# Performance work log

Hardware: AMD Instinct MI355X
Metric: run time of the kernel (lower is better)

The kernel has to match this reference:

```python
import jax, jax.numpy as jnp
import numpy as np

T = 2048      # total tokens (single prefill sequence)
HID = 2048    # hidden_size
H = 16        # num k-heads == num v-heads
DK = 128      # key head dim
DV = 128      # value head dim
K = 4         # causal conv kernel width
EPS = 1e-6


def setup_inputs() -> dict:
    key = jax.random.key(0)
    ks = jax.random.split(key, 10)
    n = lambda k, shape, sc: (jax.random.normal(k, shape, jnp.float32) * sc)
    return {
        "hidden_states": n(ks[0], (T, HID), 1.0),
        "Wq": n(ks[1], (HID, H * DK), 0.02),
        "Wk": n(ks[2], (HID, H * DK), 0.02),
        "Wv": n(ks[3], (HID, H * DV), 0.02),
        "Wb": n(ks[4], (HID, H), 0.02),
        "conv_wq": n(ks[5], (H * DK, K), 0.5),
        "conv_wk": n(ks[6], (H * DK, K), 0.5),
        "conv_wv": n(ks[7], (H * DV, K), 0.5),
        "o_norm_w": jnp.ones((DV,), jnp.float32),
        "Wo": n(ks[8], (HID, HID), 0.02),
    }


def _causal_conv_silu(x, w):
    # x: [T, D], w: [D, K] depthwise causal conv, then SiLU (matches causal_conv1d_fn)
    xp = jnp.pad(x, ((K - 1, 0), (0, 0)))
    y = sum(xp[j:j + T] * w[:, j] for j in range(K))
    return jax.nn.silu(y)


def _l2norm(x):
    return x * jax.lax.rsqrt(jnp.sum(x * x, axis=-1, keepdims=True) + EPS)


def reference(hidden_states, Wq, Wk, Wv, Wb, conv_wq, conv_wk, conv_wv, o_norm_w, Wo):
    # projections [T, H*D]
    q = _causal_conv_silu(hidden_states @ Wq, conv_wq).reshape(T, H, DK)
    k = _causal_conv_silu(hidden_states @ Wk, conv_wk).reshape(T, H, DK)
    v = _causal_conv_silu(hidden_states @ Wv, conv_wv).reshape(T, H, DV)
    beta = jax.nn.sigmoid(hidden_states @ Wb)  # [T, H]

    # qk l2-norm + scale (FLA chunk_delta_rule defaults)
    q = _l2norm(q) * (DK ** -0.5)
    k = _l2norm(k)

    # delta-rule recurrence: S <- S + beta * k (v - k^T S)
    def step(S, inp):
        q_t, k_t, v_t, b_t = inp            # [H,DK],[H,DK],[H,DV],[H]
        kS = jnp.einsum('hk,hkv->hv', k_t, S)
        delta = b_t[:, None] * (v_t - kS)   # [H, DV]
        S = S + jnp.einsum('hk,hv->hkv', k_t, delta)
        o_t = jnp.einsum('hk,hkv->hv', q_t, S)
        return S, o_t

    S0 = jnp.zeros((H, DK, DV), jnp.float32)
    _, o = jax.lax.scan(step, S0, (q, k, v, beta))  # o: [T, H, DV]

    # per-head RMSNorm on value head dim
    o = o * jax.lax.rsqrt(jnp.mean(o * o, axis=-1, keepdims=True) + EPS) * o_norm_w
    out = o.reshape(T, H * DV) @ Wo
    return out
```

## Files before the change

### kernel.cpp

```cpp
#include <hip/hip_runtime.h>

typedef unsigned short u16;
typedef __attribute__((ext_vector_type(4))) unsigned short u16x4;
typedef __attribute__((ext_vector_type(8))) unsigned short u16x8;
typedef __attribute__((ext_vector_type(8))) short short8;
typedef __attribute__((ext_vector_type(4))) float f32x4;

#define DEVI __device__ __forceinline__

DEVI u16 f2b(float f) {
  union { float f; unsigned u; } x; x.f = f;
  unsigned r = (x.u + 0x7fffu + ((x.u >> 16) & 1u)) >> 16;
  return (u16)r;
}
DEVI float b2f(u16 h) {
  union { unsigned u; float f; } x; x.u = ((unsigned)h) << 16;
  return x.f;
}
DEVI f32x4 mfma_bf16(short8 a, short8 b, f32x4 c) {
  return __builtin_amdgcn_mfma_f32_16x16x32_bf16(a, b, c, 0, 0, 0);
}
DEVI void gl2lds16(const u16* g, u16* l) {
  __builtin_amdgcn_global_load_lds((__attribute__((address_space(1))) void*)g,
                                   (__attribute__((address_space(3))) void*)l,
                                   16, 0, 0);
}
DEVI void barrier_lds() {
  asm volatile("s_waitcnt lgkmcnt(0)\n\ts_barrier" ::: "memory");
}

__global__ void k_cvt(const float* __restrict__ src, u16* __restrict__ dst, int n4,
                      const float* __restrict__ Wb, u16* __restrict__ WbT) {
  int b = blockIdx.x;
  if (b < 4096) {
    int i = b * 256 + threadIdx.x;
    if (i < n4) {
      float4 v = ((const float4*)src)[i];
      u16x4 r; r.x = f2b(v.x); r.y = f2b(v.y); r.z = f2b(v.z); r.w = f2b(v.w);
      ((u16x4*)dst)[i] = r;
    }
  } else {
    int j = (b - 4096) * 256 + threadIdx.x;
    int n = j >> 11, k = j & 2047;
    WbT[j] = f2b(Wb[k * 16 + n]);
  }
}

__global__ __launch_bounds__(256)
void k_transpose4(const float* __restrict__ s0, const float* __restrict__ s1,
                  const float* __restrict__ s2, const float* __restrict__ s3,
                  u16* __restrict__ d0, u16* __restrict__ d1,
                  u16* __restrict__ d2, u16* __restrict__ d3) {
  const int RC = 2048;
  const float* src = (blockIdx.z == 0) ? s0 : (blockIdx.z == 1) ? s1 : (blockIdx.z == 2) ? s2 : s3;
  u16* dst = (blockIdx.z == 0) ? d0 : (blockIdx.z == 1) ? d1 : (blockIdx.z == 2) ? d2 : d3;
  __shared__ u16 tile[64 * 66];
  int bx = blockIdx.x << 6, by = blockIdx.y << 6;
  int x = threadIdx.x & 63, g = threadIdx.x >> 6;
#pragma unroll
  for (int i = 0; i < 16; ++i) {
    int r = (i << 2) + g;
    tile[x * 66 + r] = f2b(src[(size_t)(by + r) * RC + bx + x]);
  }
  __syncthreads();
#pragma unroll
  for (int i = 0; i < 16; ++i) {
    int r = (i << 2) + g;
    dst[(size_t)(bx + r) * RC + by + x] = tile[r * 66 + x];
  }
}

__global__ __launch_bounds__(256, 4)
void k_gemm_bt(const u16* __restrict__ A, const u16* __restrict__ BT,
               float* __restrict__ Cf, u16* __restrict__ Cb,
               int M, int N, int K, int outbf) {
  __shared__ __align__(16) u16 As[4096];
  __shared__ __align__(16) u16 Bs[4096];
  const int tid = threadIdx.x, wave = tid >> 6, lane = tid & 63;
  const long bm = (long)blockIdx.y << 7, bn = (long)blockIdx.x << 7;
  const int r0 = (wave << 4) + (lane >> 2);
  const int kof = (((lane & 3) ^ ((lane >> 3) & 3)) << 3);
  const u16* gA = A + (bm + r0) * (long)K + kof;
  const u16* gB = BT + (bn + r0) * (long)K + kof;
  u16* lA = As + (wave << 9);
  u16* lB = Bs + (wave << 9);
  const long stepR = (long)64 * K;
  const int wr = (wave >> 1) << 6, wc = (wave & 1) << 6;
  const int fr = lane & 15, fq = (lane >> 4) << 3;
  const int fqs = fq ^ (((fr >> 1) & 3) << 3);
  f32x4 acc[4][4];
#pragma unroll
  for (int i = 0; i < 4; ++i)
#pragma unroll
    for (int j = 0; j < 4; ++j) acc[i][j] = (f32x4){0.f, 0.f, 0.f, 0.f};
  for (int k0 = 0; k0 < K; k0 += 32) {
    gl2lds16(gA + k0, lA);
    gl2lds16(gA + stepR + k0, lA + 2048);
    gl2lds16(gB + k0, lB);
    gl2lds16(gB + stepR + k0, lB + 2048);
    __syncthreads();
    short8 af[4], bfr[4];
#pragma unroll
    for (int t = 0; t < 4; ++t)
      af[t] = *(const short8*)&As[(wr + (t << 4) + fr) * 32 + fqs];
#pragma unroll
    for (int t = 0; t < 4; ++t)
      bfr[t] = *(const short8*)&Bs[(wc + (t << 4) + fr) * 32 + fqs];
#pragma unroll
    for (int i = 0; i < 4; ++i)
#pragma unroll
      for (int j = 0; j < 4; ++j)
        acc[i][j] = mfma_bf16(af[i], bfr[j], acc[i][j]);
    __syncthreads();
  }
  const int er = (lane >> 4) << 2, ec = lane & 15;
#pragma unroll
  for (int i = 0; i < 4; ++i)
#pragma unroll
    for (int j = 0; j < 4; ++j)
#pragma unroll
      for (int r = 0; r < 4; ++r) {
        long row = bm + wr + (i << 4) + er + r;
        long col = bn + wc + (j << 4) + ec;
        if (outbf) Cb[row * N + col] = f2b(acc[i][j][r]);
        else       Cf[row * N + col] = acc[i][j][r];
      }
}

__global__ __launch_bounds__(256, 4)
void k_gemm_bt64(const u16* __restrict__ A, const u16* __restrict__ BT,
                 float* __restrict__ Cf, int M, int N, int K) {
  __shared__ __align__(16) u16 As[2048];
  __shared__ __align__(16) u16 Bs[4096];
  const int tid = threadIdx.x, wave = tid >> 6, lane = tid & 63;
  const long bm = (long)blockIdx.y << 6, bn = (long)blockIdx.x << 7;
  const int r0 = (wave << 4) + (lane >> 2);
  const int kof = (((lane & 3) ^ ((lane >> 3) & 3)) << 3);
  const u16* gA = A + (bm + r0) * (long)K + kof;
  const u16* gB = BT + (bn + r0) * (long)K + kof;
  u16* lA = As + (wave << 9);
  u16* lB = Bs + (wave << 9);
  const long stepR = (long)64 * K;
  const int wr = (wave >> 1) << 5, wc = (wave & 1) << 6;
  const int fr = lane & 15, fq = (lane >> 4) << 3;
  const int fqs = fq ^ (((fr >> 1) & 3) << 3);
  f32x4 acc[2][4];
#pragma unroll
  for (int i = 0; i < 2; ++i)
#pragma unroll
    for (int j = 0; j < 4; ++j) acc[i][j] = (f32x4){0.f, 0.f, 0.f, 0.f};
  for (int k0 = 0; k0 < K; k0 += 32) {
    gl2lds16(gA + k0, lA);
    gl2lds16(gB + k0, lB);
    gl2lds16(gB + stepR + k0, lB + 2048);
    __syncthreads();
    short8 af[2], bfr[4];
#pragma unroll
    for (int t = 0; t < 2; ++t)
      af[t] = *(const short8*)&As[(wr + (t << 4) + fr) * 32 + fqs];
#pragma unroll
    for (int t = 0; t < 4; ++t)
      bfr[t] = *(const short8*)&Bs[(wc + (t << 4) + fr) * 32 + fqs];
#pragma unroll
    for (int i = 0; i < 2; ++i)
#pragma unroll
      for (int j = 0; j < 4; ++j)
        acc[i][j] = mfma_bf16(af[i], bfr[j], acc[i][j]);
    __syncthreads();
  }
  const int er = (lane >> 4) << 2, ec = lane & 15;
#pragma unroll
  for (int i = 0; i < 2; ++i)
#pragma unroll
    for (int j = 0; j < 4; ++j)
#pragma unroll
      for (int r = 0; r < 4; ++r) {
        long row = bm + wr + (i << 4) + er + r;
        long col = bn + wc + (j << 4) + ec;
        Cf[row * N + col] = acc[i][j][r];
      }
}

__global__ __launch_bounds__(256, 4)
void k_beta(const u16* __restrict__ Xb, const u16* __restrict__ WbT,
            float* __restrict__ beta) {
  __shared__ float part[4][256];
  int tid = threadIdx.x, w = tid >> 6, lane = tid & 63;
  int t0 = blockIdx.x << 4;
  int fr = lane & 15, fq = (lane >> 4) << 3;
  const u16* ap = Xb + (size_t)(t0 + fr) * 2048 + (w << 9) + fq;
  const u16* bp = WbT + (size_t)fr * 2048 + (w << 9) + fq;
  f32x4 acc = {0.f, 0.f, 0.f, 0.f};
#pragma unroll
  for (int ks = 0; ks < 16; ++ks)
    acc = mfma_bf16(*(const short8*)(ap + (ks << 5)), *(const short8*)(bp + (ks << 5)), acc);
  int er = (lane >> 4) << 2;
#pragma unroll
  for (int r = 0; r < 4; ++r) part[w][(er + r) * 16 + fr] = acc[r];
  __syncthreads();
  float s = part[0][tid] + part[1][tid] + part[2][tid] + part[3][tid];
  beta[(t0 << 4) + tid] = 1.f / (1.f + __expf(-s));
}

__global__ void k_conv(const u16* __restrict__ qkv,
                       const float* __restrict__ cwq, const float* __restrict__ cwk,
                       const float* __restrict__ cwv,
                       u16* __restrict__ qn, u16* __restrict__ kn, u16* __restrict__ vn) {
  int t = blockIdx.x, s = blockIdx.y;
  int kind = s >> 4, h = s & 15, d = threadIdx.x;
  int col = kind * 2048 + (h << 7) + d;
  const float* cw = (kind == 0) ? cwq : ((kind == 1) ? cwk : cwv);
  float4 w = *(const float4*)(cw + (size_t)((h << 7) + d) * 4);
  float x[4];
#pragma unroll
  for (int j = 0; j < 4; ++j) {
    int tt = t - 3 + j;
    x[j] = (tt >= 0) ? b2f(qkv[(size_t)tt * 6144 + col]) : 0.f;
  }
  float y = x[0] * w.x + x[1] * w.y + x[2] * w.z + x[3] * w.w;
  y = y / (1.f + __expf(-y));
  float sc = 1.f;
  __shared__ float red[2];
  if (kind < 2) {
    float ss = y * y;
#pragma unroll
    for (int off = 32; off; off >>= 1) ss += __shfl_down(ss, off, 64);
    int lane = threadIdx.x & 63, wv = threadIdx.x >> 6;
    if (lane == 0) red[wv] = ss;
    __syncthreads();
    float tot = red[0] + red[1];
    sc = rsqrtf(tot + 1e-6f);
    if (kind == 0) sc *= 0.08838834764831843f;
  }
  u16* dst = (kind == 0) ? qn : ((kind == 1) ? kn : vn);
  dst[((size_t)h << 18) + ((size_t)t << 7) + d] = f2b(y * sc);
}

__global__ __launch_bounds__(256, 2)
void k_prep(const u16* __restrict__ qn, const u16* __restrict__ kn, const u16* __restrict__ vn,
            const float* __restrict__ beta,
            u16* __restrict__ Gg, u16* __restrict__ Wg,
            u16* __restrict__ KTg, u16* __restrict__ UTg) {
  __shared__ __align__(16) char sm[70912];
  u16*  Kc  = (u16*)sm;
  u16*  Qc  = (u16*)(sm + 17408);
  u16*  Vc  = (u16*)(sm + 34816);
  u16*  KTl = (u16*)(sm + 52224);
  float* AL = (float*)(sm + 52224);
  float* Bl = (float*)(sm + 70656);
  u16*  WR  = Qc;
  int h = blockIdx.x, c = blockIdx.y;
  int tid = threadIdx.x, wave = tid >> 6, lane = tid & 63;
  size_t ch = (size_t)(c * 16 + h);
  const u16* kb = kn + ((size_t)h << 18) + ((size_t)c << 13);
  const u16* qb = qn + ((size_t)h << 18) + ((size_t)c << 13);
  const u16* vb = vn + ((size_t)h << 18) + ((size_t)c << 13);
#pragma unroll
  for (int s = 0; s < 4; ++s) {
    int e = (tid + (s << 8)) << 3;
    int t = e >> 7, d = e & 127;
    *(u16x8*)&Kc[t * 136 + d] = *(const u16x8*)(kb + e);
    *(u16x8*)&Qc[t * 136 + d] = *(const u16x8*)(qb + e);
    *(u16x8*)&Vc[t * 136 + d] = *(const u16x8*)(vb + e);
  }
  if (tid < 64) Bl[tid] = beta[((c << 6) + tid) * 16 + h];
  __syncthreads();
  int fr = lane & 15, fq = (lane >> 4) << 3, q4 = (lane >> 4) << 2;
  int arow = (wave << 4) + fr;
  f32x4 kk[4], qk[4];
#pragma unroll
  for (int ct = 0; ct < 4; ++ct) { kk[ct] = (f32x4){0.f,0.f,0.f,0.f}; qk[ct] = (f32x4){0.f,0.f,0.f,0.f}; }
#pragma unroll
  for (int ks = 0; ks < 4; ++ks) {
    short8 aK = *(const short8*)&Kc[arow * 136 + (ks << 5) + fq];
    short8 aQ = *(const short8*)&Qc[arow * 136 + (ks << 5) + fq];
#pragma unroll
    for (int ct = 0; ct < 4; ++ct) {
      short8 bK = *(const short8*)&Kc[((ct << 4) + fr) * 136 + (ks << 5) + fq];
      kk[ct] = mfma_bf16(aK, bK, kk[ct]);
      qk[ct] = mfma_bf16(aQ, bK, qk[ct]);
    }
  }
#pragma unroll
  for (int ct = 0; ct < 4; ++ct)
#pragma unroll
    for (int r = 0; r < 4; ++r) {
      int i = (wave << 4) + q4 + r, j = (ct << 4) + fr;
      Gg[(ch << 12) + i * 64 + j] = f2b((j <= i) ? qk[ct][r] : 0.f);
    }
  {
    int d = tid & 127, tg = tid >> 7;
#pragma unroll
    for (int it = 0; it < 4; ++it) {
      int t0 = (tg + (it << 1)) << 3;
      u16x8 pk;
#pragma unroll
      for (int j = 0; j < 8; ++j) pk[j] = Kc[(t0 + j) * 136 + d];
      *(u16x8*)&KTl[d * 72 + t0] = pk;
    }
  }
  __syncthreads();
#pragma unroll
  for (int it = 0; it < 4; ++it) {
    int idx = tid + (it << 8);
    int row = idx >> 3, j8 = (idx & 7) << 3;
    *(u16x8*)(KTg + (ch << 13) + (row << 6) + j8) = *(const u16x8*)&KTl[row * 72 + j8];
  }
  __syncthreads();
  {
    float bi[4];
#pragma unroll
    for (int r = 0; r < 4; ++r) bi[r] = Bl[(wave << 4) + q4 + r];
#pragma unroll
    for (int ct = 0; ct < 4; ++ct)
#pragma unroll
      for (int r = 0; r < 4; ++r) {
        int i = (wave << 4) + q4 + r, j = (ct << 4) + fr;
        AL[i * 64 + j] = (j < i) ? bi[r] * kk[ct][r] : 0.f;
      }
  }
  __syncthreads();
  float X[64];
  {
    const u16* colp = (tid < 128) ? (Kc + tid) : (Vc + (tid - 128));
#pragma unroll
    for (int t = 0; t < 64; ++t) X[t] = Bl[t] * b2f(colp[t * 136]);
#pragma unroll
    for (int r = 1; r < 64; ++r) {
      float s = 0.f;
      const float* Ar = &AL[r * 64];
      int r4 = r & ~3;
#pragma unroll
      for (int l = 0; l < 64; l += 4)
        if (l + 4 <= r) {
          float4 a = *(const float4*)(Ar + l);
          s += a.x * X[l] + a.y * X[l + 1] + a.z * X[l + 2] + a.w * X[l + 3];
        }
#pragma unroll
      for (int l = 0; l < 4; ++l)
        if (r4 + l < r) s += Ar[r4 + l] * X[r4 + l];
      X[r] -= s;
    }
  }
  __syncthreads();
  if (tid < 128) {
#pragma unroll
    for (int t = 0; t < 64; ++t) WR[t * 136 + tid] = f2b(X[t]);
  } else {
    int v = tid - 128;
    u16* dstr = UTg + (ch << 13) + (v << 6);
#pragma unroll
    for (int j = 0; j < 8; ++j) {
      u16x8 p;
#pragma unroll
      for (int e = 0; e < 8; ++e) p[e] = f2b(X[(j << 3) + e]);
      *(u16x8*)(dstr + (j << 3)) = p;
    }
  }
  __syncthreads();
#pragma unroll
  for (int it = 0; it < 4; ++it) {
    int idx = tid + (it << 8);
    int row = idx >> 4, j8 = (idx & 15) << 3;
    *(u16x8*)(Wg + (ch << 13) + (row << 7) + j8) = *(const u16x8*)&WR[row * 136 + j8];
  }
}

struct Frags { short8 q[4], w[4], g[2], k[4]; u16x4 u; };

DEVI void load_frags(Frags& f, const u16* qh, const u16* Wg, const u16* Gg,
                     const u16* KTg, const u16* UTg, int c, int h,
                     int trow, int fr, int fq, int q4, int w, int vbase) {
  const u16* qb = qh + ((size_t)((c << 6) + trow + fr) << 7) + fq;
#pragma unroll
  for (int ks = 0; ks < 4; ++ks) f.q[ks] = *(const short8*)(qb + (ks << 5));
  size_t ch = (size_t)(c * 16 + h);
  const u16* wb = Wg + (ch << 13) + ((size_t)(trow + fr) << 7) + fq;
#pragma unroll
  for (int ks = 0; ks < 4; ++ks) f.w[ks] = *(const short8*)(wb + (ks << 5));
  const u16* gb = Gg + (ch << 12) + ((size_t)(trow + fr) << 6) + fq;
#pragma unroll
  for (int ks = 0; ks < 2; ++ks) f.g[ks] = *(const short8*)(gb + (ks << 5));
  const u16* kbp = KTg + (ch << 13) + ((size_t)(w << 5) << 6) + fq;
#pragma unroll
  for (int dt = 0; dt < 2; ++dt)
#pragma unroll
    for (int ks = 0; ks < 2; ++ks)
      f.k[(dt << 1) | ks] = *(const short8*)(kbp + ((size_t)((dt << 4) + fr) << 6) + (ks << 5));
  f.u = *(const u16x4*)(UTg + (ch << 13) + ((size_t)(vbase + fr) << 6) + trow + q4);
}

DEVI void chunk_body(int c, Frags& f, u16* ST, u16* DT, u16* oh,
                     int trow, int fr, int fq, int q4, int w, int vbase,
                     f32x4& S0, f32x4& S1) {
#pragma unroll
  for (int r = 0; r < 4; ++r) {
    ST[(q4 + r) * 136 + (w << 5) + fr] = f2b(S0[r]);
    ST[(q4 + r) * 136 + (w << 5) + 16 + fr] = f2b(S1[r]);
  }
  barrier_lds();
  short8 sf[4];
#pragma unroll
  for (int ks = 0; ks < 4; ++ks) sf[ks] = *(const short8*)&ST[fr * 136 + (ks << 5) + fq];
  f32x4 racc = {0.f,0.f,0.f,0.f}, oacc = {0.f,0.f,0.f,0.f};
#pragma unroll
  for (int ks = 0; ks < 4; ++ks) {
    racc = mfma_bf16(f.w[ks], sf[ks], racc);
    oacc = mfma_bf16(f.q[ks], sf[ks], oacc);
  }
#pragma unroll
  for (int r = 0; r < 4; ++r)
    DT[fr * 72 + trow + q4 + r] = f2b(b2f(f.u[r]) - racc[r]);
  barrier_lds();
  short8 df[2];
#pragma unroll
  for (int ks = 0; ks < 2; ++ks) df[ks] = *(const short8*)&DT[fr * 72 + (ks << 5) + fq];
#pragma unroll
  for (int ks = 0; ks < 2; ++ks) {
    oacc = mfma_bf16(f.g[ks], df[ks], oacc);
    S0 = mfma_bf16(df[ks], f.k[ks], S0);
    S1 = mfma_bf16(df[ks], f.k[2 | ks], S1);
  }
#pragma unroll
  for (int r = 0; r < 4; ++r)
    oh[(size_t)((c << 6) + trow + q4 + r) * 128 + vbase + fr] = f2b(oacc[r]);
}

__global__ __launch_bounds__(256, 1)
void k_delta(const u16* __restrict__ qn, const u16* __restrict__ Wg,
             const u16* __restrict__ Gg, const u16* __restrict__ KTg,
             const u16* __restrict__ UTg, u16* __restrict__ o) {
  __shared__ __align__(16) u16 ST[16 * 136];
  __shared__ __align__(16) u16 DT[16 * 72];
  int bx = blockIdx.x;
  int h = bx & 15, vbase = (bx >> 4) << 4;
  int tid = threadIdx.x, w = tid >> 6, lane = tid & 63;
  int fr = lane & 15, fq = (lane >> 4) << 3, q4 = (lane >> 4) << 2;
  int trow = w << 4;
  const u16* qh = qn + ((size_t)h << 18);
  u16* oh = o + ((size_t)h << 18);
  f32x4 S0 = {0.f,0.f,0.f,0.f}, S1 = {0.f,0.f,0.f,0.f};
  Frags fa, fb;
  load_frags(fa, qh, Wg, Gg, KTg, UTg, 0, h, trow, fr, fq, q4, w, vbase);
  for (int c = 0; c < 32; c += 2) {
    int c1 = c + 1, c2 = (c + 2 < 32) ? c + 2 : 31;
    load_frags(fb, qh, Wg, Gg, KTg, UTg, c1, h, trow, fr, fq, q4, w, vbase);
    chunk_body(c, fa, ST, DT, oh, trow, fr, fq, q4, w, vbase, S0, S1);
    load_frags(fa, qh, Wg, Gg, KTg, UTg, c2, h, trow, fr, fq, q4, w, vbase);
    chunk_body(c1, fb, ST, DT, oh, trow, fr, fq, q4, w, vbase, S0, S1);
  }
}

__global__ void k_onorm(const u16* __restrict__ o, const float* __restrict__ onw,
                        u16* __restrict__ onb) {
  int t = blockIdx.x, h = blockIdx.y, d = threadIdx.x;
  float x = b2f(o[((size_t)h << 18) + ((size_t)t << 7) + d]);
  float ss = x * x;
#pragma unroll
  for (int off = 32; off; off >>= 1) ss += __shfl_down(ss, off, 64);
  __shared__ float red[2];
  int lane = d & 63, wv = d >> 6;
  if (lane == 0) red[wv] = ss;
  __syncthreads();
  float tot = red[0] + red[1];
  float y = x * rsqrtf(tot * (1.f / 128.f) + 1e-6f) * onw[d];
  onb[((size_t)t << 11) + (h << 7) + d] = f2b(y);
}

extern "C" void kernel_launch(void* const* d_in, const int* in_sizes, int n_in,
                              void* d_out, int out_size, void* d_ws, size_t ws_size,
                              hipStream_t stream) {
  (void)in_sizes; (void)n_in; (void)out_size; (void)ws_size;
  const float* hs  = (const float*)d_in[0];
  const float* Wq  = (const float*)d_in[1];
  const float* Wk  = (const float*)d_in[2];
  const float* Wv  = (const float*)d_in[3];
  const float* Wb  = (const float*)d_in[4];
  const float* cwq = (const float*)d_in[5];
  const float* cwk = (const float*)d_in[6];
  const float* cwv = (const float*)d_in[7];
  const float* onw = (const float*)d_in[8];
  const float* Wo  = (const float*)d_in[9];
  float* out = (float*)d_out;
  char* ws = (char*)d_ws;
  const size_t MB = 1ull << 20;
  u16*  Xb   = (u16*)(ws);
  u16*  WT   = (u16*)(ws + 8  * MB);
  u16*  WoT  = (u16*)(ws + 32 * MB);
  u16*  QKV  = (u16*)(ws + 40 * MB);
  u16*  Wg   = (u16*)(ws + 40 * MB);
  u16*  KTg  = (u16*)(ws + 48 * MB);
  u16*  UTg  = (u16*)(ws + 56 * MB);
  u16*  qn_  = (u16*)(ws + 64 * MB);
  u16*  kn_  = (u16*)(ws + 72 * MB);
  u16*  vn_  = (u16*)(ws + 80 * MB);
  float* beta= (float*)(ws + 88 * MB);
  u16*  WbT  = (u16*)(ws + 88 * MB + 512 * 1024);
  u16*  Gm   = (u16*)(ws + 89 * MB);
  u16*  o_   = (u16*)(ws + 93 * MB);
  u16*  onb  = (u16*)(ws + 109 * MB);

  k_cvt<<<4224, 256, 0, stream>>>(hs, Xb, 2048 * 2048 / 4, Wb, WbT);
  k_transpose4<<<dim3(32, 32, 4), 256, 0, stream>>>(
      Wq, Wk, Wv, Wo, WT, WT + 2048 * 2048, WT + 2 * 2048 * 2048, WoT);
  k_gemm_bt<<<dim3(48, 16), 256, 0, stream>>>(Xb, WT, nullptr, QKV, 2048, 6144, 2048, 1);
  k_beta<<<128, 256, 0, stream>>>(Xb, WbT, beta);
  k_conv<<<dim3(2048, 48), 128, 0, stream>>>(QKV, cwq, cwk, cwv, qn_, kn_, vn_);
  k_prep<<<dim3(16, 32), 256, 0, stream>>>(qn_, kn_, vn_, beta, Gm, Wg, KTg, UTg);
  k_delta<<<128, 256, 0, stream>>>(qn_, Wg, Gm, KTg, UTg, o_);
  k_onorm<<<dim3(2048, 16), 128, 0, stream>>>(o_, onw, onb);
  k_gemm_bt64<<<dim3(16, 32), 256, 0, stream>>>(onb, WoT, out, 2048, 2048, 2048);
}
```

Baseline: 374.5 us.

## Tile conv and o-norm kernels over 64 tokens; shrink Wo GEMM tile

The causal conv kernel now processes a 64-token by 128-channel tile per block. It stages the rows plus a 3-row halo in LDS once, instead of having each thread reload four scalar values, and it writes 16-byte vectorised outputs. The L2/RMS reductions shrink to 4-lane shuffles. The o-norm kernel gets the same per-thread 32-element vectorised treatment, and the Wo GEMM tile drops from 64x128 to 64x64, doubling the block count to 1024 for better CU occupancy at the cost of less operand reuse. The goal is to cut launch and scalar-memory overhead in the small elementwise kernels.

```diff
diff --git a/kernel.cpp b/kernel.cpp
--- a/kernel.cpp
+++ b/kernel.cpp
@@ -128,43 +128,40 @@
 }
 
 __global__ __launch_bounds__(256, 4)
-void k_gemm_bt64(const u16* __restrict__ A, const u16* __restrict__ BT,
-                 float* __restrict__ Cf, int M, int N, int K) {
+void k_gemm_wo(const u16* __restrict__ A, const u16* __restrict__ BT,
+               float* __restrict__ Cf, int M, int N, int K) {
   __shared__ __align__(16) u16 As[2048];
-  __shared__ __align__(16) u16 Bs[4096];
+  __shared__ __align__(16) u16 Bs[2048];
   const int tid = threadIdx.x, wave = tid >> 6, lane = tid & 63;
-  const long bm = (long)blockIdx.y << 6, bn = (long)blockIdx.x << 7;
+  const long bm = (long)blockIdx.y << 6, bn = (long)blockIdx.x << 6;
   const int r0 = (wave << 4) + (lane >> 2);
   const int kof = (((lane & 3) ^ ((lane >> 3) & 3)) << 3);
   const u16* gA = A + (bm + r0) * (long)K + kof;
   const u16* gB = BT + (bn + r0) * (long)K + kof;
   u16* lA = As + (wave << 9);
   u16* lB = Bs + (wave << 9);
-  const long stepR = (long)64 * K;
-  const int wr = (wave >> 1) << 5, wc = (wave & 1) << 6;
+  const int wr = (wave >> 1) << 5, wc = (wave & 1) << 5;
   const int fr = lane & 15, fq = (lane >> 4) << 3;
   const int fqs = fq ^ (((fr >> 1) & 3) << 3);
-  f32x4 acc[2][4];
+  f32x4 acc[2][2];
 #pragma unroll
   for (int i = 0; i < 2; ++i)
 #pragma unroll
-    for (int j = 0; j < 4; ++j) acc[i][j] = (f32x4){0.f, 0.f, 0.f, 0.f};
+    for (int j = 0; j < 2; ++j) acc[i][j] = (f32x4){0.f, 0.f, 0.f, 0.f};
   for (int k0 = 0; k0 < K; k0 += 32) {
     gl2lds16(gA + k0, lA);
     gl2lds16(gB + k0, lB);
-    gl2lds16(gB + stepR + k0, lB + 2048);
     __syncthreads();
-    short8 af[2], bfr[4];
-#pragma unroll
-    for (int t = 0; t < 2; ++t)
-      af[t] = *(const short8*)&As[(wr + (t << 4) + fr) * 32 + fqs];
-#pragma unroll
-    for (int t = 0; t < 4; ++t)
+    short8 af[2], bfr[2];
+#pragma unroll
+    for (int t = 0; t < 2; ++t) {
+      af[t]  = *(const short8*)&As[(wr + (t << 4) + fr) * 32 + fqs];
       bfr[t] = *(const short8*)&Bs[(wc + (t << 4) + fr) * 32 + fqs];
+    }
 #pragma unroll
     for (int i = 0; i < 2; ++i)
 #pragma unroll
-      for (int j = 0; j < 4; ++j)
+      for (int j = 0; j < 2; ++j)
         acc[i][j] = mfma_bf16(af[i], bfr[j], acc[i][j]);
     __syncthreads();
   }
@@ -172,7 +169,7 @@
 #pragma unroll
   for (int i = 0; i < 2; ++i)
 #pragma unroll
-    for (int j = 0; j < 4; ++j)
+    for (int j = 0; j < 2; ++j)
 #pragma unroll
       for (int r = 0; r < 4; ++r) {
         long row = bm + wr + (i << 4) + er + r;
@@ -202,38 +199,63 @@
   beta[(t0 << 4) + tid] = 1.f / (1.f + __expf(-s));
 }
 
-__global__ void k_conv(const u16* __restrict__ qkv,
-                       const float* __restrict__ cwq, const float* __restrict__ cwk,
-                       const float* __restrict__ cwv,
-                       u16* __restrict__ qn, u16* __restrict__ kn, u16* __restrict__ vn) {
-  int t = blockIdx.x, s = blockIdx.y;
-  int kind = s >> 4, h = s & 15, d = threadIdx.x;
-  int col = kind * 2048 + (h << 7) + d;
+__global__ __launch_bounds__(256, 4)
+void k_conv(const u16* __restrict__ qkv,
+            const float* __restrict__ cwq, const float* __restrict__ cwk,
+            const float* __restrict__ cwv,
+            u16* __restrict__ qn, u16* __restrict__ kn, u16* __restrict__ vn) {
+  __shared__ __align__(16) u16 xs[67 * 136];
+  __shared__ float wf[128 * 4];
+  int tt = blockIdx.x, s = blockIdx.y;
+  int kind = s >> 4, h = s & 15;
+  int t0 = tt << 6;
+  int col = (kind << 11) + (h << 7);
+  int tid = threadIdx.x;
   const float* cw = (kind == 0) ? cwq : ((kind == 1) ? cwk : cwv);
-  float4 w = *(const float4*)(cw + (size_t)((h << 7) + d) * 4);
-  float x[4];
-#pragma unroll
-  for (int j = 0; j < 4; ++j) {
-    int tt = t - 3 + j;
-    x[j] = (tt >= 0) ? b2f(qkv[(size_t)tt * 6144 + col]) : 0.f;
-  }
-  float y = x[0] * w.x + x[1] * w.y + x[2] * w.z + x[3] * w.w;
-  y = y / (1.f + __expf(-y));
+  if (tid < 128) *(float4*)&wf[tid << 2] = *(const float4*)(cw + (size_t)((h << 7) + tid) * 4);
+  for (int i = tid; i < 1072; i += 256) {
+    int prow = i >> 4, c8 = (i & 15) << 3;
+    int g = t0 - 3 + prow;
+    u16x8 v = {0, 0, 0, 0, 0, 0, 0, 0};
+    if (g >= 0) v = *(const u16x8*)(qkv + (size_t)g * 6144 + col + c8);
+    *(u16x8*)&xs[prow * 136 + c8] = v;
+  }
+  __syncthreads();
+  int t = tid >> 2, dg = tid & 3;
+  float y[32];
+  float ss = 0.f;
+#pragma unroll
+  for (int e8 = 0; e8 < 4; ++e8) {
+    int d0 = (dg << 5) + (e8 << 3);
+    u16x8 a0 = *(const u16x8*)&xs[(t + 0) * 136 + d0];
+    u16x8 a1 = *(const u16x8*)&xs[(t + 1) * 136 + d0];
+    u16x8 a2 = *(const u16x8*)&xs[(t + 2) * 136 + d0];
+    u16x8 a3 = *(const u16x8*)&xs[(t + 3) * 136 + d0];
+#pragma unroll
+    for (int e = 0; e < 8; ++e) {
+      float4 w = *(const float4*)&wf[(d0 + e) << 2];
+      float v = b2f(a0[e]) * w.x + b2f(a1[e]) * w.y + b2f(a2[e]) * w.z + b2f(a3[e]) * w.w;
+      v = v / (1.f + __expf(-v));
+      y[(e8 << 3) + e] = v;
+      ss += v * v;
+    }
+  }
   float sc = 1.f;
-  __shared__ float red[2];
   if (kind < 2) {
-    float ss = y * y;
-#pragma unroll
-    for (int off = 32; off; off >>= 1) ss += __shfl_down(ss, off, 64);
-    int lane = threadIdx.x & 63, wv = threadIdx.x >> 6;
-    if (lane == 0) red[wv] = ss;
-    __syncthreads();
-    float tot = red[0] + red[1];
-    sc = rsqrtf(tot + 1e-6f);
+    ss += __shfl_xor(ss, 1);
+    ss += __shfl_xor(ss, 2);
+    sc = rsqrtf(ss + 1e-6f);
     if (kind == 0) sc *= 0.08838834764831843f;
   }
   u16* dst = (kind == 0) ? qn : ((kind == 1) ? kn : vn);
-  dst[((size_t)h << 18) + ((size_t)t << 7) + d] = f2b(y * sc);
+  u16* dp = dst + ((size_t)h << 18) + ((size_t)(t0 + t) << 7) + (dg << 5);
+#pragma unroll
+  for (int e8 = 0; e8 < 4; ++e8) {
+    u16x8 p;
+#pragma unroll
+    for (int e = 0; e < 8; ++e) p[e] = f2b(y[(e8 << 3) + e] * sc);
+    *(u16x8*)(dp + (e8 << 3)) = p;
+  }
 }
 
 __global__ __launch_bounds__(256, 2)
@@ -451,20 +473,35 @@
   }
 }
 
-__global__ void k_onorm(const u16* __restrict__ o, const float* __restrict__ onw,
-                        u16* __restrict__ onb) {
-  int t = blockIdx.x, h = blockIdx.y, d = threadIdx.x;
-  float x = b2f(o[((size_t)h << 18) + ((size_t)t << 7) + d]);
-  float ss = x * x;
-#pragma unroll
-  for (int off = 32; off; off >>= 1) ss += __shfl_down(ss, off, 64);
-  __shared__ float red[2];
-  int lane = d & 63, wv = d >> 6;
-  if (lane == 0) red[wv] = ss;
-  __syncthreads();
-  float tot = red[0] + red[1];
-  float y = x * rsqrtf(tot * (1.f / 128.f) + 1e-6f) * onw[d];
-  onb[((size_t)t << 11) + (h << 7) + d] = f2b(y);
+__global__ __launch_bounds__(256, 4)
+void k_onorm(const u16* __restrict__ o, const float* __restrict__ onw,
+             u16* __restrict__ onb) {
+  __shared__ float wl[128];
+  int tt = blockIdx.x, h = blockIdx.y, tid = threadIdx.x;
+  if (tid < 128) wl[tid] = onw[tid];
+  __syncthreads();
+  int t = tid >> 2, dg = tid & 3;
+  const u16* src = o + ((size_t)h << 18) + ((size_t)((tt << 6) + t) << 7) + (dg << 5);
+  u16x8 a[4];
+  float ss = 0.f;
+#pragma unroll
+  for (int e8 = 0; e8 < 4; ++e8) {
+    a[e8] = *(const u16x8*)(src + (e8 << 3));
+#pragma unroll
+    for (int e = 0; e < 8; ++e) { float x = b2f(a[e8][e]); ss += x * x; }
+  }
+  ss += __shfl_xor(ss, 1);
+  ss += __shfl_xor(ss, 2);
+  float inv = rsqrtf(ss * (1.f / 128.f) + 1e-6f);
+  u16* dp = onb + ((size_t)((tt << 6) + t) << 11) + (h << 7) + (dg << 5);
+#pragma unroll
+  for (int e8 = 0; e8 < 4; ++e8) {
+    u16x8 p;
+#pragma unroll
+    for (int e = 0; e < 8; ++e)
+      p[e] = f2b(b2f(a[e8][e]) * inv * wl[(dg << 5) + (e8 << 3) + e]);
+    *(u16x8*)(dp + (e8 << 3)) = p;
+  }
 }
 
 extern "C" void kernel_launch(void* const* d_in, const int* in_sizes, int n_in,
@@ -505,9 +542,9 @@
       Wq, Wk, Wv, Wo, WT, WT + 2048 * 2048, WT + 2 * 2048 * 2048, WoT);
   k_gemm_bt<<<dim3(48, 16), 256, 0, stream>>>(Xb, WT, nullptr, QKV, 2048, 6144, 2048, 1);
   k_beta<<<128, 256, 0, stream>>>(Xb, WbT, beta);
-  k_conv<<<dim3(2048, 48), 128, 0, stream>>>(QKV, cwq, cwk, cwv, qn_, kn_, vn_);
+  k_conv<<<dim3(32, 48), 256, 0, stream>>>(QKV, cwq, cwk, cwv, qn_, kn_, vn_);
   k_prep<<<dim3(16, 32), 256, 0, stream>>>(qn_, kn_, vn_, beta, Gm, Wg, KTg, UTg);
   k_delta<<<128, 256, 0, stream>>>(qn_, Wg, Gm, KTg, UTg, o_);
-  k_onorm<<<dim3(2048, 16), 128, 0, stream>>>(o_, onw, onb);
-  k_gemm_bt64<<<dim3(16, 32), 256, 0, stream>>>(onb, WoT, out, 2048, 2048, 2048);
-}
+  k_onorm<<<dim3(32, 16), 256, 0, stream>>>(o_, onw, onb);
+  k_gemm_wo<<<dim3(32, 32), 256, 0, stream>>>(onb, WoT, out, 2048, 2048, 2048);
+}
```

After: 347.0 us. -7.4%, faster.
